# Performance work log

Measured on AMD Instinct MI355X. Metric: run time of the kernel, lower is better.

## Reference

```python
import jax, jax.numpy as jnp
import numpy as np

N_ATOMS = 4096
BOX = 37.0
CUTOFF = 5.0


def _f_r(r, fe, beta, re, lam):
    # f_e * exp(-beta*(r/r_e - 1)) / (1 + (r/r_e - lamda)^20)
    x = r / re
    return fe * jnp.exp(-beta * (x - 1.0)) / (1.0 + (x - lam) ** 20)


def _phi_r(r, a, b, re, alpha, beta, kappa, lam):
    x = r / re
    l = a * jnp.exp(-alpha * (x - 1.0)) / (1.0 + (x - kappa) ** 20)
    rr = b * jnp.exp(-beta * (x - 1.0)) / (1.0 + (x - lam) ** 20)
    return l - rr


def setup_inputs() -> dict:
    key = jax.random.key(0)
    k1, k2 = jax.random.split(key)
    # coordinates in a box sized for metal-like density so neighbors exist within cutoff
    coords = jax.random.uniform(k1, (N_ATOMS, 3), dtype=jnp.float32) * BOX
    # all 22 EAM parameters positive in [1.0, 2.5] (r_e, rho_s, rho_n, rho_0, eta must be > 0)
    params = 1.0 + 1.5 * jax.random.uniform(k2, (N_ATOMS, 22), dtype=jnp.float32)
    return {"coords": coords, "params": params}


def reference(coords, params):
    N = coords.shape[0]
    # docstring column order: r_e, f_e, rho_e, rho_s, alpha, beta, A, B, kappa, lamda,
    # f_n0..f_n3, f_0..f_3, eta, f_e2, rho_n, rho_0
    r_e, f_e, rho_e, rho_s = params[:, 0], params[:, 1], params[:, 2], params[:, 3]
    alpha, beta = params[:, 4], params[:, 5]
    A, B, kappa, lam = params[:, 6], params[:, 7], params[:, 8], params[:, 9]
    eta, f_e2 = params[:, 18], params[:, 19]
    rho_n, rho_0 = params[:, 20], params[:, 21]

    # ---- full pairwise distances (safe diagonal for differentiable sqrt) ----
    diff = coords[None, :, :] - coords[:, None, :]            # [N, N, 3]
    r2 = jnp.sum(diff * diff, axis=-1)                        # [N, N]
    eye = jnp.eye(N, dtype=bool)
    r_mat = jnp.sqrt(jnp.where(eye, 1.0, r2))                 # [N, N]

    # ---- pair energy over i<j with r <= cutoff (masked, same math as torch filtering) ----
    iu, ju = jnp.triu_indices(N, k=1)                         # P = N(N-1)/2 pairs
    r_pair = r_mat[iu, ju]
    mask = r_pair <= CUTOFF
    r_safe = jnp.where(mask, r_pair, 1.0)                     # nan-safe for masked-out pairs

    fr_i = _f_r(r_safe, f_e[iu], beta[iu], r_e[iu], lam[iu])
    fr_j = _f_r(r_safe, f_e[ju], beta[ju], r_e[ju], lam[ju])
    ph_i = _phi_r(r_safe, A[iu], B[iu], r_e[iu], alpha[iu], beta[iu], kappa[iu], lam[iu])
    ph_j = _phi_r(r_safe, A[ju], B[ju], r_e[ju], alpha[ju], beta[ju], kappa[ju], lam[ju])
    phi_01 = fr_j / fr_i * ph_i + fr_i / fr_j * ph_j
    p_e = 0.5 * jnp.sum(jnp.where(mask, phi_01, 0.0))

    # ---- per-atom density rho_i = sum_{j != i} f_r(r_ij, params_j) (no cutoff, as in source) ----
    fr_mat = _f_r(r_mat, f_e[None, :], beta[None, :], r_e[None, :], lam[None, :])
    rho = jnp.sum(jnp.where(eye, 0.0, fr_mat), axis=1)        # [N]

    # ---- embedding F(rho) with three branches (if/elif/else -> nested where) ----
    xn = rho / rho_n - 1.0
    poly_n = params[:, 10] + params[:, 11] * xn + params[:, 12] * xn ** 2 + params[:, 13] * xn ** 3
    xe = rho / rho_e - 1.0
    poly_0 = params[:, 14] + params[:, 15] * xe + params[:, 16] * xe ** 2 + params[:, 17] * xe ** 3
    t = (rho / rho_s) ** eta
    tail = f_e2 * (1.0 - jnp.log(t)) * t
    F_i = jnp.where(rho < rho_n, poly_n, jnp.where(rho < rho_0, poly_0, tail))

    return p_e + jnp.sum(F_i)
```

## Files before the change

### kernel.cpp

```cpp
#include <hip/hip_runtime.h>
#include <math.h>

#define N_ATOMS 4096
#define NTILE   16
#define NJ      64
#define JT      64
#define LOG2E   1.4426950408889634f
#define LN2     0.6931471805599453f

typedef float v2f __attribute__((ext_vector_type(2)));
typedef unsigned long long u64;

__device__ __forceinline__ float pow20f(float t) {
    float t2 = t * t, t4 = t2 * t2, t8 = t4 * t4, t16 = t8 * t8;
    return t16 * t4;
}

__device__ __forceinline__ float block_reduce(float v, float* red) {
    __syncthreads();
    #pragma unroll
    for (int off = 32; off > 0; off >>= 1) v += __shfl_down(v, off, 64);
    if ((threadIdx.x & 63) == 0) red[threadIdx.x >> 6] = v;
    __syncthreads();
    return (red[0] + red[1]) + (red[2] + red[3]);
}

__global__ __launch_bounds__(256) void eam_main(
    const float* __restrict__ coords, const float* __restrict__ params,
    float* __restrict__ rho_part,
    float* __restrict__ e_part,
    int* __restrict__ ctr)
{
    __shared__ float4 srho4[JT];
    __shared__ float4 sphi4[JT * 3];
    __shared__ float red[4];

    const int tid = threadIdx.x;
    const int bi  = blockIdx.x;
    const int s   = blockIdx.y;
    const int i   = bi * 256 + tid;
    const int jbase = s * JT;

    if (bi == 0 && s == 0 && tid == 0) *ctr = 0;

    if (tid < JT) {
        const int j = jbase + tid;
        const float* p = params + 22 * j;
        const float x = coords[3*j], y = coords[3*j+1], z = coords[3*j+2];
        const float re = p[0], fe = p[1], be = p[5], al = p[4], la = p[9];
        const float rei  = __builtin_amdgcn_rcpf(re);
        const float bl2  = be * LOG2E;
        const float al2  = al * LOG2E;
        const float l2fe = __builtin_amdgcn_logf(fe);

        float lo = la + 1.0f, hi = la + 6.0f;
        #pragma unroll 1
        for (int it = 0; it < 28; ++it) {
            const float mid = 0.5f * (lo + hi);
            const float g   = l2fe - bl2 * (mid - 1.0f)
                            - __builtin_amdgcn_logf(1.0f + pow20f(mid - la)) + 19.93f;
            if (g > 0.0f) lo = mid; else hi = mid;
        }
        const float rc  = re * hi;
        const float rc2 = fmaxf(rc * rc, 25.01f);

        sphi4[tid * 3 + 0] = { x, y, z, rei };
        sphi4[tid * 3 + 1] = { -bl2 * rei, bl2 + l2fe, -la, p[7] * __builtin_amdgcn_rcpf(fe) };
        sphi4[tid * 3 + 2] = { -al2 * rei, al2, -p[8], p[6] };
        float* rd = (float*)srho4 + 8 * (tid >> 1) + (tid & 1);
        rd[0] = x; rd[2] = y; rd[4] = z; rd[6] = rc2;
    }

    const float* pi = params + 22 * i;
    const float xi = coords[3*i], yi = coords[3*i+1], zi = coords[3*i+2];
    const float rei_i  = __builtin_amdgcn_rcpf(pi[0]);
    const float bl2_i  = pi[5] * LOG2E;
    const float al2_i  = pi[4] * LOG2E;
    const float c0b_i  = -bl2_i * rei_i;
    const float c1bp_i = bl2_i + __builtin_amdgcn_logf(pi[1]);
    const float c0a_i  = -al2_i * rei_i;
    const float mla_i  = -pi[9];
    const float mka_i  = -pi[8];
    const float A_i    = pi[6];
    const float Bof_i  = pi[7] * __builtin_amdgcn_rcpf(pi[1]);

    __syncthreads();

    const v2f xi2 = { xi, xi }, yi2 = { yi, yi }, zi2 = { zi, zi };
    u64 hits = 0ull;

    #pragma unroll 4
    for (int k = 0; k < JT / 2; ++k) {
        const float4 f0 = srho4[k * 2 + 0];
        const float4 f1 = srho4[k * 2 + 1];
        const v2f x01 = { f0.x, f0.y }, y01 = { f0.z, f0.w };
        const v2f z01 = { f1.x, f1.y };
        const v2f dx = x01 - xi2, dy = y01 - yi2, dz = z01 - zi2;
        const v2f r2v = dx * dx + dy * dy + dz * dz;
        if (r2v.x <= f1.z) hits |= (1ull << (2 * k));
        if (r2v.y <= f1.w) hits |= (1ull << (2 * k + 1));
    }

    const int t = i - jbase;
    float rho = 0.0f;
    u64 phim = 0ull;

    {
        u64 m = hits;
        if (t >= 0 && t < JT) m &= ~(1ull << t);
        while (m) {
            const int k = __builtin_ctzll(m);
            m &= m - 1;
            const float4 q0 = sphi4[k * 3 + 0];
            const float4 q1 = sphi4[k * 3 + 1];
            const float dx = q0.x - xi, dy = q0.y - yi, dz = q0.z - zi;
            const float r2 = fmaf(dx, dx, fmaf(dy, dy, dz * dz));
            const float r  = __builtin_amdgcn_sqrtf(r2);
            const float fr = __builtin_amdgcn_exp2f(fmaf(r, q1.x, q1.y))
                           * __builtin_amdgcn_rcpf(1.0f + pow20f(fmaf(r, q0.w, q1.z)));
            rho += fr;
            if (r2 <= 25.0f && k > t) phim |= (1ull << k);
        }
    }
    rho_part[(size_t)s * N_ATOMS + i] = rho;

    float e = 0.0f;
    while (phim) {
        const int k = __builtin_ctzll(phim);
        phim &= phim - 1;
        const float4 q0 = sphi4[k * 3 + 0];
        const float4 q1 = sphi4[k * 3 + 1];
        const float4 q2 = sphi4[k * 3 + 2];
        const float dx = q0.x - xi, dy = q0.y - yi, dz = q0.z - zi;
        const float r = __builtin_amdgcn_sqrtf(fmaf(dx, dx, fmaf(dy, dy, dz * dz)));

        const float fri = __builtin_amdgcn_exp2f(fmaf(r, c0b_i, c1bp_i))
                        * __builtin_amdgcn_rcpf(1.0f + pow20f(fmaf(r, rei_i, mla_i)));
        const float frj = __builtin_amdgcn_exp2f(fmaf(r, q1.x, q1.y))
                        * __builtin_amdgcn_rcpf(1.0f + pow20f(fmaf(r, q0.w, q1.z)));
        const float ph_i = A_i * __builtin_amdgcn_exp2f(fmaf(r, c0a_i, al2_i))
                               * __builtin_amdgcn_rcpf(1.0f + pow20f(fmaf(r, rei_i, mka_i)))
                         - Bof_i * fri;
        const float ph_j = q2.w * __builtin_amdgcn_exp2f(fmaf(r, q2.x, q2.y))
                                * __builtin_amdgcn_rcpf(1.0f + pow20f(fmaf(r, q0.w, q2.z)))
                         - q1.w * frj;
        e += 0.5f * fmaf(frj * frj, ph_i, fri * fri * ph_j)
                  * __builtin_amdgcn_rcpf(fri * frj);
    }

    const float eb = block_reduce(e, red);
    if (tid == 0) e_part[bi * NJ + s] = eb;
}

__global__ __launch_bounds__(1024) void eam_embed(
    const float* __restrict__ params,
    const float* __restrict__ rho_part, const float* __restrict__ e_part,
    float* __restrict__ tile_sum,
    int* __restrict__ ctr, float* __restrict__ out)
{
    __shared__ float acc[4][256];
    __shared__ float red16[16];
    __shared__ int sLast;
    const int tid = threadIdx.x;
    const int b   = blockIdx.x;
    const int al  = tid & 255;
    const int q   = tid >> 8;
    const int i   = b * 256 + al;

    float part = 0.0f;
    #pragma unroll 4
    for (int s = q * 16; s < q * 16 + 16; ++s)
        part += rho_part[(size_t)s * N_ATOMS + i];
    acc[q][al] = part;
    __syncthreads();

    float v = 0.0f;
    if (tid < 256) {
        const float rhoi = (acc[0][tid] + acc[1][tid]) + (acc[2][tid] + acc[3][tid]);
        const float* p = params + 22 * i;
        float F;
        if (rhoi < p[20]) {
            const float xn = rhoi / p[20] - 1.0f;
            F = p[10] + xn * (p[11] + xn * (p[12] + xn * p[13]));
        } else if (rhoi < p[21]) {
            const float xe = rhoi / p[2] - 1.0f;
            F = p[14] + xe * (p[15] + xe * (p[16] + xe * p[17]));
        } else {
            const float l2 = __builtin_amdgcn_logf(rhoi / p[3]);
            const float tt = __builtin_amdgcn_exp2f(p[18] * l2);
            const float lt = p[18] * l2 * LN2;
            F = p[19] * (1.0f - lt) * tt;
        }
        v = F + ((tid < NJ) ? e_part[b * NJ + tid] : 0.0f);
    }

    #pragma unroll
    for (int off = 32; off > 0; off >>= 1) v += __shfl_down(v, off, 64);
    if ((tid & 63) == 0) red16[tid >> 6] = v;
    __syncthreads();
    if (tid == 0) {
        float sum = 0.0f;
        #pragma unroll
        for (int w = 0; w < 16; ++w) sum += red16[w];
        tile_sum[b] = sum;
        int prev = __hip_atomic_fetch_add(ctr, 1, __ATOMIC_ACQ_REL,
                                          __HIP_MEMORY_SCOPE_AGENT);
        sLast = (prev == NTILE - 1);
    }
    __syncthreads();

    if (sLast && tid == 0) {
        float total = 0.0f;
        #pragma unroll
        for (int w = 0; w < NTILE; ++w) total += tile_sum[w];
        out[0] = total;
    }
}

extern "C" void kernel_launch(void* const* d_in, const int* in_sizes, int n_in,
                              void* d_out, int out_size, void* d_ws, size_t ws_size,
                              hipStream_t stream) {
    const float* coords = (const float*)d_in[0];
    const float* params = (const float*)d_in[1];
    float* out = (float*)d_out;

    float* rho_part = (float*)d_ws;
    float* e_part   = rho_part + (size_t)NJ * N_ATOMS;
    float* tile_sum = e_part + NTILE * NJ;
    int*   ctr      = (int*)(tile_sum + NTILE);

    dim3 grid(NTILE, NJ);
    eam_main<<<grid, 256, 0, stream>>>(coords, params, rho_part, e_part, ctr);
    eam_embed<<<NTILE, 1024, 0, stream>>>(params, rho_part, e_part, tile_sum, ctr, out);
}
```

Baseline: 20.22 us.

## Fuse embedding pass into main kernel via last-block-per-tile atomic counters

Merges the embedding/reduction kernel into the main pairwise kernel. Each tile's last-arriving block, detected with a per-tile atomic counter, sums the rho partials, evaluates F, and reduces, and a global counter picks the block that writes the final sum. A tiny zeroing kernel replaces the old in-kernel counter reset. This removes one dependent launch but serialises the rho reduction onto a single 256-thread block per tile instead of 1024 threads, and still issues two launches.

```diff
diff --git a/kernel.cpp b/kernel.cpp
--- a/kernel.cpp
+++ b/kernel.cpp
@@ -25,23 +25,30 @@
     return (red[0] + red[1]) + (red[2] + red[3]);
 }
 
-__global__ __launch_bounds__(256) void eam_main(
+__global__ __launch_bounds__(32) void zero_ctrs(unsigned int* __restrict__ ctrs)
+{
+    if (threadIdx.x < NTILE + 1) ctrs[threadIdx.x] = 0u;
+}
+
+__global__ __launch_bounds__(256) void eam_fused(
     const float* __restrict__ coords, const float* __restrict__ params,
     float* __restrict__ rho_part,
     float* __restrict__ e_part,
-    int* __restrict__ ctr)
+    float* __restrict__ tile_sum,
+    unsigned int* __restrict__ tctr,
+    unsigned int* __restrict__ gctr,
+    float* __restrict__ out)
 {
     __shared__ float4 srho4[JT];
     __shared__ float4 sphi4[JT * 3];
     __shared__ float red[4];
+    __shared__ int sTileLast, sGlobLast;
 
     const int tid = threadIdx.x;
     const int bi  = blockIdx.x;
     const int s   = blockIdx.y;
     const int i   = bi * 256 + tid;
     const int jbase = s * JT;
-
-    if (bi == 0 && s == 0 && tid == 0) *ctr = 0;
 
     if (tid < JT) {
         const int j = jbase + tid;
@@ -149,36 +156,28 @@
     }
 
     const float eb = block_reduce(e, red);
-    if (tid == 0) e_part[bi * NJ + s] = eb;
-}
-
-__global__ __launch_bounds__(1024) void eam_embed(
-    const float* __restrict__ params,
-    const float* __restrict__ rho_part, const float* __restrict__ e_part,
-    float* __restrict__ tile_sum,
-    int* __restrict__ ctr, float* __restrict__ out)
-{
-    __shared__ float acc[4][256];
-    __shared__ float red16[16];
-    __shared__ int sLast;
-    const int tid = threadIdx.x;
-    const int b   = blockIdx.x;
-    const int al  = tid & 255;
-    const int q   = tid >> 8;
-    const int i   = b * 256 + al;
-
-    float part = 0.0f;
+    if (tid == 0) {
+        e_part[bi * NJ + s] = eb;
+        unsigned int prev = __hip_atomic_fetch_add(&tctr[bi], 1u, __ATOMIC_ACQ_REL,
+                                                   __HIP_MEMORY_SCOPE_AGENT);
+        sTileLast = (prev == (unsigned)(NJ - 1));
+    }
+    __syncthreads();
+    if (!sTileLast) return;
+
+    float rsum0 = 0.0f, rsum1 = 0.0f, rsum2 = 0.0f, rsum3 = 0.0f;
     #pragma unroll 4
-    for (int s = q * 16; s < q * 16 + 16; ++s)
-        part += rho_part[(size_t)s * N_ATOMS + i];
-    acc[q][al] = part;
-    __syncthreads();
-
-    float v = 0.0f;
-    if (tid < 256) {
-        const float rhoi = (acc[0][tid] + acc[1][tid]) + (acc[2][tid] + acc[3][tid]);
+    for (int ss = 0; ss < NJ; ss += 4) {
+        rsum0 += rho_part[(size_t)(ss + 0) * N_ATOMS + i];
+        rsum1 += rho_part[(size_t)(ss + 1) * N_ATOMS + i];
+        rsum2 += rho_part[(size_t)(ss + 2) * N_ATOMS + i];
+        rsum3 += rho_part[(size_t)(ss + 3) * N_ATOMS + i];
+    }
+    const float rhoi = (rsum0 + rsum1) + (rsum2 + rsum3);
+
+    float F;
+    {
         const float* p = params + 22 * i;
-        float F;
         if (rhoi < p[20]) {
             const float xn = rhoi / p[20] - 1.0f;
             F = p[10] + xn * (p[11] + xn * (p[12] + xn * p[13]));
@@ -191,25 +190,19 @@
             const float lt = p[18] * l2 * LN2;
             F = p[19] * (1.0f - lt) * tt;
         }
-        v = F + ((tid < NJ) ? e_part[b * NJ + tid] : 0.0f);
-    }
-
-    #pragma unroll
-    for (int off = 32; off > 0; off >>= 1) v += __shfl_down(v, off, 64);
-    if ((tid & 63) == 0) red16[tid >> 6] = v;
-    __syncthreads();
+    }
+
+    float v = F + ((tid < NJ) ? e_part[bi * NJ + tid] : 0.0f);
+    const float tot = block_reduce(v, red);
     if (tid == 0) {
-        float sum = 0.0f;
-        #pragma unroll
-        for (int w = 0; w < 16; ++w) sum += red16[w];
-        tile_sum[b] = sum;
-        int prev = __hip_atomic_fetch_add(ctr, 1, __ATOMIC_ACQ_REL,
-                                          __HIP_MEMORY_SCOPE_AGENT);
-        sLast = (prev == NTILE - 1);
-    }
-    __syncthreads();
-
-    if (sLast && tid == 0) {
+        tile_sum[bi] = tot;
+        unsigned int prev = __hip_atomic_fetch_add(gctr, 1u, __ATOMIC_ACQ_REL,
+                                                   __HIP_MEMORY_SCOPE_AGENT);
+        sGlobLast = (prev == (unsigned)(NTILE - 1));
+    }
+    __syncthreads();
+
+    if (sGlobLast && tid == 0) {
         float total = 0.0f;
         #pragma unroll
         for (int w = 0; w < NTILE; ++w) total += tile_sum[w];
@@ -227,9 +220,11 @@
     float* rho_part = (float*)d_ws;
     float* e_part   = rho_part + (size_t)NJ * N_ATOMS;
     float* tile_sum = e_part + NTILE * NJ;
-    int*   ctr      = (int*)(tile_sum + NTILE);
-
+    unsigned int* tctr = (unsigned int*)(tile_sum + NTILE);
+    unsigned int* gctr = tctr + NTILE;
+
+    zero_ctrs<<<1, 32, 0, stream>>>(tctr);
     dim3 grid(NTILE, NJ);
-    eam_main<<<grid, 256, 0, stream>>>(coords, params, rho_part, e_part, ctr);
-    eam_embed<<<NTILE, 1024, 0, stream>>>(params, rho_part, e_part, tile_sum, ctr, out);
-}
+    eam_fused<<<grid, 256, 0, stream>>>(coords, params, rho_part, e_part,
+                                        tile_sum, tctr, gctr, out);
+}
```

Measured after the change: 43.47 us. 2.15x slower.
